# Kernel tuning notes

Measured on AMD Instinct MI355X. Metric: run time of the kernel, lower is better.

## Reference

```python
import jax, jax.numpy as jnp
import numpy as np


def setup_inputs() -> dict:
    key = jax.random.key(0)
    ks = jax.random.split(key, 5)
    N, D, H, E = 4096, 1024, 4096, 8
    x = jax.random.normal(ks[0], (N, D), dtype=jnp.float32)
    gate_w = jax.random.normal(ks[1], (D, E), dtype=jnp.float32) * (1.0 / np.sqrt(D))
    gate_b = jnp.zeros((E,), dtype=jnp.float32)
    W1 = jax.random.normal(ks[2], (E, D, H), dtype=jnp.float32) * (1.0 / np.sqrt(D))
    b1 = jnp.zeros((E, H), dtype=jnp.float32)
    W2 = jax.random.normal(ks[3], (E, H, D), dtype=jnp.float32) * (1.0 / np.sqrt(H))
    b2 = jnp.zeros((E, D), dtype=jnp.float32)
    return {"x": x, "gate_w": gate_w, "gate_b": gate_b,
            "W1": W1, "b1": b1, "W2": W2, "b2": b2}


def reference(x, gate_w, gate_b, W1, b1, W2, b2):
    # x: [N, D]; W1: [E, D, H]; W2: [E, H, D]
    K = 2
    N, D = x.shape
    E = gate_w.shape[1]
    logits = x @ gate_w + gate_b                      # [N, E]
    probs = jax.nn.softmax(logits, axis=-1)           # [N, E]
    topw, topi = jax.lax.top_k(probs, K)              # [N, K] each; raw probs, not renormalized
    # combine weights as dense [N, E] (zero for unselected experts)
    combine = jnp.zeros((N, E), dtype=x.dtype).at[jnp.arange(N)[:, None], topi].add(topw)
    # batched expert MLP over all experts (dense-dispatch; math identical to top-k combine)
    h = jnp.einsum('nd,edh->enh', x, W1) + b1[:, None, :]   # [E, N, H]
    h = jax.nn.gelu(h, approximate=True)                     # tanh-approx GELU
    y = jnp.einsum('enh,ehd->end', h, W2) + b2[:, None, :]   # [E, N, D]
    out = jnp.einsum('end,ne->nd', y, combine)               # weighted combine
    return out
```

## Files before the change

### kernel.cpp

```cpp
#include <hip/hip_runtime.h>
#include <cstdint>
#include <cstddef>

#define DEVI __device__ __forceinline__

constexpr int N_TOK = 4096, DIM = 1024, HID = 4096, NE = 8;
constexpr int NKR = N_TOK * 2;

typedef __attribute__((ext_vector_type(8))) short short8;
typedef __attribute__((ext_vector_type(4))) float f32x4;

DEVI ushort f2bf(float f) {
  union { float f; uint32_t u; } v; v.f = f;
  uint32_t r = v.u + 0x7FFFu + ((v.u >> 16) & 1u);
  return (ushort)(r >> 16);
}

DEVI float gelu_t(float x) {
  float t = 0.7978845608028654f * (x + 0.044715f * x * x * x);
  t = fminf(fmaxf(t, -15.f), 15.f);
  float e = __expf(2.f * t);
  return 0.5f * x * (1.f + (e - 1.f) / (e + 1.f));
}

DEVI void gload_lds16(const ushort* g, ushort* l) {
  __builtin_amdgcn_global_load_lds(
      (const __attribute__((address_space(1))) void*)g,
      (__attribute__((address_space(3))) void*)l, 16, 0, 0);
}

__global__ void convert_x_kernel(const float* __restrict__ x, ushort* __restrict__ xbf) {
  int i = (blockIdx.x * 256 + threadIdx.x) * 4;
  float4 v = *(const float4*)(x + i);
  ushort4 o;
  o.x = f2bf(v.x); o.y = f2bf(v.y); o.z = f2bf(v.z); o.w = f2bf(v.w);
  *(ushort4*)(xbf + i) = o;
}

template<int R, int C>
__global__ void transpose_bf16(const float* __restrict__ src, ushort* __restrict__ dst) {
  __shared__ ushort t[64][68];
  int e = blockIdx.z;
  const float* s = src + (size_t)e * R * C;
  ushort* d = dst + (size_t)e * R * C;
  int r0 = blockIdx.y * 64, c0 = blockIdx.x * 64;
  int lr = threadIdx.x >> 4;
  int lc = (threadIdx.x & 15) * 4;
#pragma unroll
  for (int i = 0; i < 4; ++i) {
    int r = lr + i * 16;
    float4 v = *(const float4*)(s + (size_t)(r0 + r) * C + c0 + lc);
    t[lc + 0][r] = f2bf(v.x);
    t[lc + 1][r] = f2bf(v.y);
    t[lc + 2][r] = f2bf(v.z);
    t[lc + 3][r] = f2bf(v.w);
  }
  __syncthreads();
#pragma unroll
  for (int i = 0; i < 4; ++i) {
    int c = lr + i * 16;
    ushort4 o = *(const ushort4*)&t[c][lc];
    *(ushort4*)(d + (size_t)(c0 + c) * R + r0 + lc) = o;
  }
}

__global__ void gate_kernel(const float* __restrict__ x, const float* __restrict__ gw,
                            const float* __restrict__ gb,
                            int* __restrict__ topi, float* __restrict__ topw,
                            int* __restrict__ counts) {
  int n = blockIdx.x;
  int lane = threadIdx.x;
  double p[NE];
#pragma unroll
  for (int e = 0; e < NE; ++e) p[e] = 0.0;
  const float* xr = x + (size_t)n * DIM;
  for (int d = lane; d < DIM; d += 64) {
    float xv = xr[d];
    const float* g = gw + (size_t)d * NE;
#pragma unroll
    for (int e = 0; e < NE; ++e) p[e] += (double)xv * (double)g[e];
  }
#pragma unroll
  for (int e = 0; e < NE; ++e) {
#pragma unroll
    for (int s = 32; s > 0; s >>= 1) p[e] += __shfl_down(p[e], s);
  }
  if (lane == 0) {
    double m = -1e300;
#pragma unroll
    for (int e = 0; e < NE; ++e) { p[e] += (double)gb[e]; if (p[e] > m) m = p[e]; }
    double s = 0.0, ex[NE];
#pragma unroll
    for (int e = 0; e < NE; ++e) { ex[e] = exp(p[e] - m); s += ex[e]; }
    double inv = 1.0 / s;
    int e0 = 0, e1 = 0; double v0 = -1.0, v1 = -1.0;
#pragma unroll
    for (int e = 0; e < NE; ++e) {
      double pe = ex[e] * inv;
      if (pe > v0)      { v1 = v0; e1 = e0; v0 = pe; e0 = e; }
      else if (pe > v1) { v1 = pe; e1 = e; }
    }
    topi[n * 2] = e0; topi[n * 2 + 1] = e1;
    topw[n * 2] = (float)v0; topw[n * 2 + 1] = (float)v1;
    atomicAdd(&counts[e0], 1);
    atomicAdd(&counts[e1], 1);
  }
}

__global__ void prefix_kernel(const int* __restrict__ counts, int* __restrict__ offs) {
  if (threadIdx.x == 0) {
    int s = 0;
    for (int e = 0; e < NE; ++e) { offs[e] = s; s += counts[e]; }
  }
}

__global__ void scatter_kernel(const int* __restrict__ topi, const float* __restrict__ topw,
                               const int* __restrict__ offs, int* __restrict__ fill,
                               int* __restrict__ tok, float* __restrict__ wgt) {
  int n = blockIdx.x * blockDim.x + threadIdx.x;
  if (n >= N_TOK) return;
#pragma unroll
  for (int k = 0; k < 2; ++k) {
    int e = topi[n * 2 + k];
    int pos = atomicAdd(&fill[e], 1);
    int g = offs[e] + pos;
    tok[g] = n;
    wgt[g] = topw[n * 2 + k];
  }
}

template<int K, int NXT, int KS, bool FIRST>
__global__ __launch_bounds__(512, 2) void moe_gemm(
    const ushort* __restrict__ A,
    const ushort* __restrict__ B,
    const float* __restrict__ bias,
    const int* __restrict__ tok, const float* __restrict__ wgt,
    const int* __restrict__ offs, const int* __restrict__ counts,
    ushort* __restrict__ hbuf, float* __restrict__ out)
{
  constexpr int NCOL = FIRST ? HID : DIM;
  constexpr int KB = K / KS;
  constexpr int NK = KB / 64;
  constexpr int TSZ = 256 * 64;
  __shared__ ushort Asm[2 * TSZ];
  __shared__ ushort Bsm[2 * TSZ];

  const int bid = blockIdx.x;
  const int e   = bid & 7;
  const int rem = bid >> 3;
  const int yt  = rem & 15;
  const int xt  = (rem >> 4) % NXT;
  const int ksp = rem / (16 * NXT);

  const int cnt = counts[e];
  const int mbase = yt * 256;
  if (mbase >= cnt) return;
  const int off = offs[e];
  const int nbase = xt * 256;
  int rv = cnt - mbase; if (rv > 256) rv = 256;

  const int tid = threadIdx.x;
  const int lane = tid & 63, wave = tid >> 6;
  const int sr = tid >> 3;
  const int sc = (tid & 7) * 8;
  const int k0base = ksp * KB;

  const ushort* arow[4];
  const ushort* brow[4];
  const ushort* Be = B + (size_t)e * ((size_t)HID * DIM) + (size_t)nbase * K;
#pragma unroll
  for (int i = 0; i < 4; ++i) {
    int r = sr + 64 * i;
    int rc = r < rv ? r : rv - 1;
    int g = off + mbase + rc;
    long t = FIRST ? (long)tok[g] : (long)g;
    arow[i] = A + t * (long)K + k0base + sc;
    brow[i] = Be + (size_t)r * K + k0base + sc;
  }

  f32x4 acc[8][4];
#pragma unroll
  for (int a = 0; a < 8; ++a)
#pragma unroll
    for (int b = 0; b < 4; ++b) acc[a][b] = (f32x4)0.f;

  const int quad = lane >> 4, lrow = lane & 15;
  const int WM = (wave >> 2) * 128;
  const int WN = (wave & 3) * 64;

  auto stage = [&](int buf, int k0) {
#pragma unroll
    for (int i = 0; i < 4; ++i) {
      gload_lds16(arow[i] + k0, &Asm[buf * TSZ + (i * 64 + wave * 8) * 64]);
      gload_lds16(brow[i] + k0, &Bsm[buf * TSZ + (i * 64 + wave * 8) * 64]);
    }
  };
  auto compute = [&](int buf) {
#pragma unroll
    for (int ks = 0; ks < 2; ++ks) {
      short8 af[8], bf[4];
#pragma unroll
      for (int mt = 0; mt < 8; ++mt)
        af[mt] = *(const short8*)&Asm[buf * TSZ + (WM + mt * 16 + lrow) * 64 + ks * 32 + quad * 8];
#pragma unroll
      for (int nt = 0; nt < 4; ++nt)
        bf[nt] = *(const short8*)&Bsm[buf * TSZ + (WN + nt * 16 + lrow) * 64 + ks * 32 + quad * 8];
#pragma unroll
      for (int mt = 0; mt < 8; ++mt)
#pragma unroll
        for (int nt = 0; nt < 4; ++nt)
          acc[mt][nt] = __builtin_amdgcn_mfma_f32_16x16x32_bf16(af[mt], bf[nt], acc[mt][nt], 0, 0, 0);
    }
  };

  stage(0, 0);
  int cur = 0;
  for (int t = 0; t + 1 < NK; ++t) {
    stage(cur ^ 1, (t + 1) * 64);
    asm volatile("s_waitcnt vmcnt(8)" ::: "memory");
    __builtin_amdgcn_s_barrier();
    __builtin_amdgcn_sched_barrier(0);
    compute(cur);
    __builtin_amdgcn_sched_barrier(0);
    __builtin_amdgcn_s_barrier();
    cur ^= 1;
  }
  __syncthreads();
  compute(cur);

  if (FIRST) {
#pragma unroll
    for (int mt = 0; mt < 8; ++mt) {
#pragma unroll
      for (int i = 0; i < 4; ++i) {
        int mm = WM + mt * 16 + quad * 4 + i;
        if (mm >= rv) continue;
        size_t g = (size_t)(off + mbase + mm);
#pragma unroll
        for (int nt = 0; nt < 4; ++nt) {
          int col = nbase + WN + nt * 16 + lrow;
          float v = gelu_t(acc[mt][nt][i] + bias[e * NCOL + col]);
          hbuf[g * HID + col] = f2bf(v);
        }
      }
    }
  } else {
#pragma unroll
    for (int mt = 0; mt < 8; ++mt) {
#pragma unroll
      for (int i = 0; i < 4; ++i) {
        int mm = WM + mt * 16 + quad * 4 + i;
        if (mm >= rv) continue;
        int g = off + mbase + mm;
        long t = tok[g];
        float w = wgt[g];
#pragma unroll
        for (int nt = 0; nt < 4; ++nt) {
          int col = nbase + WN + nt * 16 + lrow;
          float bb = (ksp == 0) ? bias[e * NCOL + col] : 0.f;
          float v = w * (acc[mt][nt][i] + bb);
          atomicAdd(out + t * DIM + col, v);
        }
      }
    }
  }
}

extern "C" void kernel_launch(void* const* d_in, const int* in_sizes, int n_in,
                              void* d_out, int out_size, void* d_ws, size_t ws_size,
                              hipStream_t stream) {
  const float* x  = (const float*)d_in[0];
  const float* gw = (const float*)d_in[1];
  const float* gb = (const float*)d_in[2];
  const float* W1 = (const float*)d_in[3];
  const float* b1 = (const float*)d_in[4];
  const float* W2 = (const float*)d_in[5];
  const float* b2 = (const float*)d_in[6];
  float* out = (float*)d_out;

  char* ws = (char*)d_ws;
  size_t o = 0;
  auto alloc = [&](size_t b) { char* p = ws + o; o = (o + b + 255) & ~(size_t)255; return p; };
  int*    tok  = (int*)alloc(NKR * 4);
  float*  wgt  = (float*)alloc(NKR * 4);
  int*    topi = (int*)alloc(N_TOK * 2 * 4);
  float*  topw = (float*)alloc(N_TOK * 2 * 4);
  int*    counts = (int*)alloc(2 * NE * 4);
  int*    fill = counts + NE;
  int*    offs = (int*)alloc(NE * 4);
  ushort* xbf  = (ushort*)alloc((size_t)N_TOK * DIM * 2);
  ushort* hbuf = (ushort*)alloc((size_t)NKR * HID * 2);
  ushort* Wt   = (ushort*)alloc((size_t)NE * HID * DIM * 2);
  size_t need = o;

  hipMemsetAsync(out, 0, (size_t)out_size * sizeof(float), stream);
  if (ws_size < need) return;

  hipMemsetAsync(counts, 0, 2 * NE * 4, stream);

  convert_x_kernel<<<(N_TOK * DIM / 4) / 256, 256, 0, stream>>>(x, xbf);
  gate_kernel<<<N_TOK, 64, 0, stream>>>(x, gw, gb, topi, topw, counts);
  prefix_kernel<<<1, 64, 0, stream>>>(counts, offs);
  scatter_kernel<<<(N_TOK + 255) / 256, 256, 0, stream>>>(topi, topw, offs, fill, tok, wgt);

  transpose_bf16<DIM, HID><<<dim3(HID / 64, DIM / 64, NE), 256, 0, stream>>>(W1, Wt);
  moe_gemm<DIM, HID / 256, 1, true ><<<dim3(16 * (HID / 256) * 1 * NE), 512, 0, stream>>>(
      xbf, Wt, b1, tok, wgt, offs, counts, hbuf, out);

  transpose_bf16<HID, DIM><<<dim3(DIM / 64, HID / 64, NE), 256, 0, stream>>>(W2, Wt);
  moe_gemm<HID, DIM / 256, 2, false><<<dim3(16 * (DIM / 256) * 2 * NE), 512, 0, stream>>>(
      hbuf, Wt, b2, tok, wgt, offs, counts, hbuf, out);
}
```

Baseline: 933.6 us.

## Swizzle LDS tiles and interleave chunked staging with MFMA phases

Permutes each thread's global column chunk with an XOR pattern so tiles land swizzled in LDS, and reads fragments with the matching XOR offset. The goal is to avoid bank conflicts on the 128-byte row stride. The main loop is split into four MFMA phases, each with its own barriers and raised wave priority. The next tile's global-to-LDS loads are issued one chunk per phase instead of all at once. This adds more barriers per iteration, which may cost some synchronisation overhead.

```diff
diff --git a/kernel.cpp b/kernel.cpp
--- a/kernel.cpp
+++ b/kernel.cpp
@@ -141,9 +141,9 @@
   constexpr int NCOL = FIRST ? HID : DIM;
   constexpr int KB = K / KS;
   constexpr int NK = KB / 64;
-  constexpr int TSZ = 256 * 64;
-  __shared__ ushort Asm[2 * TSZ];
-  __shared__ ushort Bsm[2 * TSZ];
+  constexpr int TSZB = 256 * 64 * 2;
+  __shared__ ushort Asm[2 * 256 * 64];
+  __shared__ ushort Bsm[2 * 256 * 64];
 
   const int bid = blockIdx.x;
   const int e   = bid & 7;
@@ -162,7 +162,7 @@
   const int tid = threadIdx.x;
   const int lane = tid & 63, wave = tid >> 6;
   const int sr = tid >> 3;
-  const int sc = (tid & 7) * 8;
+  const int scs = (((lane & 7) ^ (lane >> 3)) * 8);
   const int k0base = ksp * KB;
 
   const ushort* arow[4];
@@ -174,8 +174,8 @@
     int rc = r < rv ? r : rv - 1;
     int g = off + mbase + rc;
     long t = FIRST ? (long)tok[g] : (long)g;
-    arow[i] = A + t * (long)K + k0base + sc;
-    brow[i] = Be + (size_t)r * K + k0base + sc;
+    arow[i] = A + t * (long)K + k0base + scs;
+    brow[i] = Be + (size_t)r * K + k0base + scs;
   }
 
   f32x4 acc[8][4];
@@ -188,45 +188,86 @@
   const int WM = (wave >> 2) * 128;
   const int WN = (wave & 3) * 64;
 
-  auto stage = [&](int buf, int k0) {
-#pragma unroll
-    for (int i = 0; i < 4; ++i) {
-      gload_lds16(arow[i] + k0, &Asm[buf * TSZ + (i * 64 + wave * 8) * 64]);
-      gload_lds16(brow[i] + k0, &Bsm[buf * TSZ + (i * 64 + wave * 8) * 64]);
+  int rowA[8], rowB[4], xo[2];
+#pragma unroll
+  for (int mt = 0; mt < 8; ++mt) rowA[mt] = (WM + mt * 16 + lrow) * 128;
+#pragma unroll
+  for (int nt = 0; nt < 4; ++nt) rowB[nt] = (WN + nt * 16 + lrow) * 128;
+#pragma unroll
+  for (int ks = 0; ks < 2; ++ks) xo[ks] = ((ks * 4 + quad) ^ (lane & 7)) * 16;
+
+#define STAGE_CHUNK(P)                                                         \
+  { gload_lds16(arow[P] + kn, (ushort*)(An + ((P) * 64 + wave * 8) * 128));    \
+    gload_lds16(brow[P] + kn, (ushort*)(Bn + ((P) * 64 + wave * 8) * 128)); }
+#define LD_AF(MH, KSX)                                                         \
+  { _Pragma("unroll") for (int j = 0; j < 4; ++j)                              \
+      af[j] = *(const short8*)(A0 + rowA[(MH) * 4 + j] + xo[KSX]); }
+#define LD_BF(KSX)                                                             \
+  { _Pragma("unroll") for (int j = 0; j < 4; ++j)                              \
+      bfr[j] = *(const short8*)(B0 + rowB[j] + xo[KSX]); }
+#define MFMA16(MH)                                                             \
+  { _Pragma("unroll") for (int j = 0; j < 4; ++j)                              \
+      _Pragma("unroll") for (int nt = 0; nt < 4; ++nt)                         \
+        acc[(MH) * 4 + j][nt] = __builtin_amdgcn_mfma_f32_16x16x32_bf16(       \
+            af[j], bfr[nt], acc[(MH) * 4 + j][nt], 0, 0, 0); }
+
+  {
+    char* An = (char*)Asm; char* Bn = (char*)Bsm; const int kn = 0;
+    STAGE_CHUNK(0); STAGE_CHUNK(1); STAGE_CHUNK(2); STAGE_CHUNK(3);
+  }
+
+  for (int t = 0; t < NK; ++t) {
+    const int cb = t & 1;
+    const char* A0 = (const char*)Asm + cb * TSZB;
+    const char* B0 = (const char*)Bsm + cb * TSZB;
+    char* An = (char*)Asm + (cb ^ 1) * TSZB;
+    char* Bn = (char*)Bsm + (cb ^ 1) * TSZB;
+    const int kn = (t + 1) * 64;
+    const bool more = (t + 1 < NK);
+    short8 af[4], bfr[4];
+
+    if (more) {
+      STAGE_CHUNK(0);
+      asm volatile("s_waitcnt vmcnt(2)" ::: "memory");
+    } else {
+      asm volatile("s_waitcnt vmcnt(0)" ::: "memory");
     }
-  };
-  auto compute = [&](int buf) {
-#pragma unroll
-    for (int ks = 0; ks < 2; ++ks) {
-      short8 af[8], bf[4];
-#pragma unroll
-      for (int mt = 0; mt < 8; ++mt)
-        af[mt] = *(const short8*)&Asm[buf * TSZ + (WM + mt * 16 + lrow) * 64 + ks * 32 + quad * 8];
-#pragma unroll
-      for (int nt = 0; nt < 4; ++nt)
-        bf[nt] = *(const short8*)&Bsm[buf * TSZ + (WN + nt * 16 + lrow) * 64 + ks * 32 + quad * 8];
-#pragma unroll
-      for (int mt = 0; mt < 8; ++mt)
-#pragma unroll
-        for (int nt = 0; nt < 4; ++nt)
-          acc[mt][nt] = __builtin_amdgcn_mfma_f32_16x16x32_bf16(af[mt], bf[nt], acc[mt][nt], 0, 0, 0);
-    }
-  };
-
-  stage(0, 0);
-  int cur = 0;
-  for (int t = 0; t + 1 < NK; ++t) {
-    stage(cur ^ 1, (t + 1) * 64);
-    asm volatile("s_waitcnt vmcnt(8)" ::: "memory");
-    __builtin_amdgcn_s_barrier();
-    __builtin_amdgcn_sched_barrier(0);
-    compute(cur);
-    __builtin_amdgcn_sched_barrier(0);
-    __builtin_amdgcn_s_barrier();
-    cur ^= 1;
-  }
-  __syncthreads();
-  compute(cur);
+    __builtin_amdgcn_s_barrier();
+    __builtin_amdgcn_sched_barrier(0);
+    LD_AF(0, 0); LD_BF(0);
+    __builtin_amdgcn_s_setprio(1); MFMA16(0); __builtin_amdgcn_s_setprio(0);
+    __builtin_amdgcn_sched_barrier(0);
+    __builtin_amdgcn_s_barrier();
+
+    LD_AF(1, 0);
+    if (more) STAGE_CHUNK(1);
+    __builtin_amdgcn_s_barrier();
+    __builtin_amdgcn_sched_barrier(0);
+    __builtin_amdgcn_s_setprio(1); MFMA16(1); __builtin_amdgcn_s_setprio(0);
+    __builtin_amdgcn_sched_barrier(0);
+    __builtin_amdgcn_s_barrier();
+
+    LD_AF(0, 1); LD_BF(1);
+    if (more) STAGE_CHUNK(2);
+    __builtin_amdgcn_s_barrier();
+    __builtin_amdgcn_sched_barrier(0);
+    __builtin_amdgcn_s_setprio(1); MFMA16(0); __builtin_amdgcn_s_setprio(0);
+    __builtin_amdgcn_sched_barrier(0);
+    __builtin_amdgcn_s_barrier();
+
+    LD_AF(1, 1);
+    if (more) STAGE_CHUNK(3);
+    __builtin_amdgcn_s_barrier();
+    __builtin_amdgcn_sched_barrier(0);
+    __builtin_amdgcn_s_setprio(1); MFMA16(1); __builtin_amdgcn_s_setprio(0);
+    __builtin_amdgcn_sched_barrier(0);
+    __builtin_amdgcn_s_barrier();
+  }
+
+#undef STAGE_CHUNK
+#undef LD_AF
+#undef LD_BF
+#undef MFMA16
 
   if (FIRST) {
 #pragma unroll
```

Result: faster. 869.1 us (-6.9%).
